# Optimization experiments

Hardware: AMD Instinct MI355X
Metric: run time of the kernel (lower is better)

The kernel has to match this reference:

```python
import jax, jax.numpy as jnp
import numpy as np

B, N, D, H, DH = 1, 1024, 512, 16, 32
NBINS, KIT = 68, 20
NEG = jnp.float32(-1e9)


def _ln(x, g, b):
    mu = jnp.mean(x, -1, keepdims=True)
    var = jnp.mean((x - mu) ** 2, -1, keepdims=True)
    return (x - mu) * jax.lax.rsqrt(var + 1e-5) * g + b


def _heads(x, W):
    b, n, _ = x.shape
    return (x @ W).reshape(b, n, H, DH).transpose(0, 2, 1, 3)  # (B,H,N,DH)


def _forward(h, x_res, pos_bins, mask, ln_mha_g, ln_mha_b, w_q, w_k, w_v, w_g, w_o,
             pos_w, ln_ff_g, ln_ff_b, sw_w1, sw_w3, sw_w2, ln_sink_g, ln_sink_b,
             w_q_sink, w_k_sink, alpha_h, r_h, eps, ln_gate_g, ln_gate_b,
             w_gate_w, w_gate_b, lambda_h_raw):
    b, n, d = h.shape
    mcol = mask[:, None, None, :] > 0  # key-side mask (B,1,1,N)
    mrow = mask[:, None, :, None] > 0

    # ---- MHA with positional bias (flash_diff_attn reference math) ----
    h_n = _ln(h, ln_mha_g, ln_mha_b)
    Q = _heads(h_n, w_q)
    K = _heads(h_n, w_k)
    V = _heads(h_n, w_v)
    G = h_n @ w_g  # (B,N,D) gate, per-head view is equivalent flattened
    bias = pos_w[pos_bins].transpose(0, 3, 1, 2)  # (B,N,N,H) -> (B,H,N,N)
    logits = jnp.einsum('bhnd,bhmd->bhnm', Q, K) / np.float32(np.sqrt(DH)) + bias
    logits = jnp.where(mcol, logits, NEG)
    P = jax.nn.softmax(logits, axis=-1)
    att = jnp.einsum('bhnm,bhmd->bhnd', P, V).transpose(0, 2, 1, 3).reshape(b, n, d)
    h = h + jax.nn.sigmoid(G) * (att @ w_o) * mask[..., None]

    # ---- SwiGLU FFN ----
    h_f = _ln(h, ln_ff_g, ln_ff_b)
    ff = (jax.nn.silu(h_f @ sw_w1) * (h_f @ sw_w3)) @ sw_w2
    h = h + ff * mask[..., None]

    # ---- Balanced Sinkhorn OT transport over coordinates ----
    h_s = _ln(h, ln_sink_g, ln_sink_b)
    Qs = _heads(h_s, w_q_sink)
    Ks = _heads(h_s, w_k_sink)
    Qs = Qs / jnp.clip(jnp.linalg.norm(Qs, axis=-1, keepdims=True), 1e-12)
    Ks = Ks / jnp.clip(jnp.linalg.norm(Ks, axis=-1, keepdims=True), 1e-12)
    sim = jnp.einsum('bhnd,bhmd->bhnm', Qs, Ks)  # cosine similarity
    # Gibbs log-kernel: higher (r_h*sim + alpha_h) => lower cost, scaled by per-head eps
    logKmat = (r_h[:, None, None] * sim + alpha_h[:, None, None]) / eps[:, None, None]
    logKmat = jnp.where(mcol, logKmat, NEG)
    logKmat = jnp.where(mrow, logKmat, NEG)
    n_valid = jnp.sum(mask, -1, keepdims=True)  # (B,1)
    log_a = jnp.where(mask > 0, -jnp.log(n_valid), NEG)[:, None, :]  # (B,1,N) uniform marginal

    def sink_step(carry, _):
        f, g = carry
        f = log_a - jax.nn.logsumexp(logKmat + g[..., None, :], axis=-1)
        g = log_a - jax.nn.logsumexp(logKmat + f[..., None], axis=-2)
        return (f, g), None

    f0 = jnp.zeros((b, H, n), h.dtype)
    (f, g), _ = jax.lax.scan(sink_step, (f0, f0), None, length=KIT)
    logP = f[..., None] + logKmat + g[..., None, :]
    Pn = jax.nn.softmax(logP, axis=-1)  # barycentric row-normalized plan
    x_cent = jnp.einsum('bhnm,bmc->bhnc', Pn, x_res)  # (B,H,N,3)
    vec_h = x_cent - x_res[:, None]

    gate = jax.nn.sigmoid(_ln(h, ln_gate_g, ln_gate_b) @ w_gate_w + w_gate_b)  # (B,N,1)
    lam = (jnp.tanh(lambda_h_raw) / H).reshape(1, H, 1, 1)
    disp = jnp.sum(lam * vec_h, axis=1)  # (B,N,3)
    x_out = x_res + gate * disp * mask[..., None]
    return h, x_out


def setup_inputs() -> dict:
    key = jax.random.key(0)
    ks = jax.random.split(key, 16)
    w = lambda k, s: (0.02 * jax.random.normal(k, s)).astype(jnp.float32)
    nr = H // 4
    return {
        'h': jax.random.normal(ks[0], (B, N, D), jnp.float32),
        'x_res': jax.random.normal(ks[1], (B, N, 3), jnp.float32),
        'pos_bins': jax.random.randint(ks[2], (B, N, N), 0, NBINS),
        'mask': jnp.ones((B, N), jnp.float32),
        'ln_mha_g': jnp.ones(D), 'ln_mha_b': jnp.zeros(D),
        'w_q': w(ks[3], (D, D)), 'w_k': w(ks[4], (D, D)), 'w_v': w(ks[5], (D, D)),
        'w_g': w(ks[6], (D, D)), 'w_o': w(ks[7], (D, D)),
        'pos_w': w(ks[8], (NBINS, H)),
        'ln_ff_g': jnp.ones(D), 'ln_ff_b': jnp.zeros(D),
        'sw_w1': w(ks[9], (D, 4 * D)), 'sw_w3': w(ks[10], (D, 4 * D)),
        'sw_w2': w(ks[11], (4 * D, D)),
        'ln_sink_g': jnp.ones(D), 'ln_sink_b': jnp.zeros(D),
        'w_q_sink': w(ks[12], (D, D)), 'w_k_sink': w(ks[13], (D, D)),
        'alpha_h': jnp.full((H,), -1.0, jnp.float32),
        'r_h': jnp.full((H,), 10.0, jnp.float32),
        'eps': jnp.asarray([0.5] * nr + [1.0] * nr + [2.0] * nr + [4.0] * nr, jnp.float32),
        'ln_gate_g': jnp.ones(D), 'ln_gate_b': jnp.zeros(D),
        'w_gate_w': w(ks[14], (D, 1)), 'w_gate_b': jnp.zeros(1),
        'lambda_h_raw': jnp.zeros(H, jnp.float32),
    }


def reference(h, x_res, pos_bins, mask, ln_mha_g, ln_mha_b, w_q, w_k, w_v, w_g, w_o,
              pos_w, ln_ff_g, ln_ff_b, sw_w1, sw_w3, sw_w2, ln_sink_g, ln_sink_b,
              w_q_sink, w_k_sink, alpha_h, r_h, eps, ln_gate_g, ln_gate_b,
              w_gate_w, w_gate_b, lambda_h_raw):
    return _forward(h, x_res, pos_bins, mask, ln_mha_g, ln_mha_b, w_q, w_k, w_v, w_g,
                    w_o, pos_w, ln_ff_g, ln_ff_b, sw_w1, sw_w3, sw_w2, ln_sink_g,
                    ln_sink_b, w_q_sink, w_k_sink, alpha_h, r_h, eps, ln_gate_g,
                    ln_gate_b, w_gate_w, w_gate_b, lambda_h_raw)
```

## Files before the change

### kernel.cpp

```cpp
#include <hip/hip_runtime.h>
#include <hip/hip_bf16.h>
#include <hip/hip_fp16.h>
#include <math.h>

#define NTOK 1024
#define DMODEL 512
#define NHEAD 16
#define DHEAD 32
#define DFF 2048
#define NBINS 68
#define KIT 20
#define NEGV (-1e9f)
#define NEGH (-30000.0f)

typedef __attribute__((ext_vector_type(8))) short bf16x8;
typedef __attribute__((ext_vector_type(4))) float f32x4;
typedef __attribute__((ext_vector_type(8))) unsigned short u16x8;

__device__ inline unsigned short f2bf(float f) {
    unsigned int u = __float_as_uint(f);
    unsigned int r = (u + 0x7fff + ((u >> 16) & 1)) >> 16;
    return (unsigned short)r;
}

__device__ inline float wave_max64(float v) {
    #pragma unroll
    for (int s = 32; s; s >>= 1) v = fmaxf(v, __shfl_xor(v, s, 64));
    return v;
}
__device__ inline float wave_sum64(float v) {
    #pragma unroll
    for (int s = 32; s; s >>= 1) v += __shfl_xor(v, s, 64);
    return v;
}

__global__ void prep_kernel(const float* __restrict__ w_q, const float* __restrict__ w_k,
                            const float* __restrict__ w_v, const float* __restrict__ w_g,
                            const float* __restrict__ w_o, const float* __restrict__ w_qs,
                            const float* __restrict__ w_ks, const float* __restrict__ sw1,
                            const float* __restrict__ sw3, const float* __restrict__ sw2,
                            unsigned short* __restrict__ wt_qkvg, unsigned short* __restrict__ wt_o,
                            unsigned short* __restrict__ wt_qsks, unsigned short* __restrict__ wt_13,
                            unsigned short* __restrict__ wt_2,
                            const float* __restrict__ mask, float* __restrict__ nv,
                            float* __restrict__ la, float* __restrict__ gv) {
    __shared__ float red[256];
    __shared__ float T[32][33];
    int b = blockIdx.x, tid = threadIdx.x;
    if (b >= 4864) {
        red[tid] = mask[tid] + mask[tid + 256] + mask[tid + 512] + mask[tid + 768];
        __syncthreads();
        for (int off = 128; off; off >>= 1) { if (tid < off) red[tid] += red[tid + off]; __syncthreads(); }
        float lognv = __logf(red[0]);
        if (tid == 0) nv[0] = red[0];
        for (int i = tid; i < NTOK; i += 256) la[i] = (mask[i] > 0.f) ? -lognv : NEGV;
        for (int i = tid; i < NHEAD * NTOK; i += 256) gv[i] = 0.f;
        return;
    }
    const float* W; unsigned short* D; int K, N, t;
    if (b < 1792) {
        int which = b >> 8; t = b & 255; K = 512; N = 512;
        switch (which) {
            case 0: W = w_q;  D = wt_qkvg; break;
            case 1: W = w_k;  D = wt_qkvg + 512 * 512; break;
            case 2: W = w_v;  D = wt_qkvg + 2 * 512 * 512; break;
            case 3: W = w_g;  D = wt_qkvg + 3 * 512 * 512; break;
            case 4: W = w_o;  D = wt_o; break;
            case 5: W = w_qs; D = wt_qsks; break;
            default: W = w_ks; D = wt_qsks + 512 * 512; break;
        }
    } else if (b < 2816) { W = sw1; D = wt_13;              K = 512;  N = 2048; t = b - 1792; }
    else if (b < 3840)   { W = sw3; D = wt_13 + 2048 * 512; K = 512;  N = 2048; t = b - 2816; }
    else                 { W = sw2; D = wt_2;               K = 2048; N = 512;  t = b - 3840; }
    int nx = N >> 5;
    int n0 = (t % nx) * 32, k0 = (t / nx) * 32;
    int r = tid >> 3, c0 = (tid & 7) * 4;
    float4 v4 = *(const float4*)&W[(size_t)(k0 + r) * N + n0 + c0];
    T[r][c0] = v4.x; T[r][c0 + 1] = v4.y; T[r][c0 + 2] = v4.z; T[r][c0 + 3] = v4.w;
    __syncthreads();
    ushort4 o;
    o.x = f2bf(T[c0][r]); o.y = f2bf(T[c0 + 1][r]);
    o.z = f2bf(T[c0 + 2][r]); o.w = f2bf(T[c0 + 3][r]);
    *(ushort4*)&D[(size_t)(n0 + r) * K + k0 + c0] = o;
}

__global__ void ln_bf16_kernel(const float* __restrict__ x, const float* __restrict__ gm,
                               const float* __restrict__ bt, unsigned short* __restrict__ out) {
    int n = blockIdx.x;
    int tid = threadIdx.x;
    __shared__ float red[256];
    const float* row = x + (size_t)n * DMODEL;
    float a = row[tid], b = row[tid + 256];
    red[tid] = a + b;
    __syncthreads();
    for (int off = 128; off; off >>= 1) { if (tid < off) red[tid] += red[tid + off]; __syncthreads(); }
    float mu = red[0] * (1.0f / DMODEL);
    __syncthreads();
    float d0 = a - mu, d1 = b - mu;
    red[tid] = d0 * d0 + d1 * d1;
    __syncthreads();
    for (int off = 128; off; off >>= 1) { if (tid < off) red[tid] += red[tid + off]; __syncthreads(); }
    float rstd = rsqrtf(red[0] * (1.0f / DMODEL) + 1e-5f);
    out[(size_t)n * DMODEL + tid]       = f2bf(d0 * rstd * gm[tid] + bt[tid]);
    out[(size_t)n * DMODEL + tid + 256] = f2bf(d1 * rstd * gm[tid + 256] + bt[tid + 256]);
}

template<int GATED>
__global__ void res_ln_kernel(const float* __restrict__ base, const __half* __restrict__ Gh,
                              const float* __restrict__ t1, const float* __restrict__ mask,
                              const float* __restrict__ gm, const float* __restrict__ bt,
                              float* __restrict__ hout, unsigned short* __restrict__ lnout) {
    int n = blockIdx.x, tid = threadIdx.x;
    __shared__ float red[256];
    float mk = mask[n];
    size_t off = (size_t)n * DMODEL;
    float a, b;
    if (GATED) {
        float g0 = __half2float(Gh[off + tid]);
        float g1 = __half2float(Gh[off + tid + 256]);
        a = base[off + tid]       + g0 * t1[off + tid]       * mk;
        b = base[off + tid + 256] + g1 * t1[off + tid + 256] * mk;
    } else {
        a = base[off + tid]       + t1[off + tid]       * mk;
        b = base[off + tid + 256] + t1[off + tid + 256] * mk;
    }
    hout[off + tid] = a; hout[off + tid + 256] = b;
    red[tid] = a + b;
    __syncthreads();
    for (int o2 = 128; o2; o2 >>= 1) { if (tid < o2) red[tid] += red[tid + o2]; __syncthreads(); }
    float mu = red[0] * (1.0f / DMODEL);
    __syncthreads();
    float d0 = a - mu, d1 = b - mu;
    red[tid] = d0 * d0 + d1 * d1;
    __syncthreads();
    for (int o2 = 128; o2; o2 >>= 1) { if (tid < o2) red[tid] += red[tid + o2]; __syncthreads(); }
    float rstd = rsqrtf(red[0] * (1.0f / DMODEL) + 1e-5f);
    lnout[off + tid]       = f2bf(d0 * rstd * gm[tid] + bt[tid]);
    lnout[off + tid + 256] = f2bf(d1 * rstd * gm[tid + 256] + bt[tid + 256]);
}

template<int MODE>
__global__ __launch_bounds__(256)
void mfma_gemm(const unsigned short* __restrict__ A, const unsigned short* __restrict__ Bt,
               float* __restrict__ C, __half* __restrict__ Ch, unsigned short* __restrict__ Cb,
               unsigned short* __restrict__ P2, unsigned short* __restrict__ P3,
               int N, int K, int lda, int ldb, int ldc,
               long sA, long sB, long sC,
               const float* __restrict__ alpha, const float* __restrict__ epsv,
               const float* __restrict__ mask) {
    __shared__ unsigned short As[128 * 64];
    __shared__ unsigned short Bs[128 * 64];
    const int h = blockIdx.z;
    A += (size_t)h * sA; Bt += (size_t)h * sB;
    const int tid = threadIdx.x;
    const int lane = tid & 63, wid = tid >> 6;
    const int wr = wid >> 1, wc = wid & 1;
    const int lr = lane & 15, kg = lane >> 4;
    const int row0 = blockIdx.y * 128, col0 = blockIdx.x * 128;
    f32x4 acc[4][4];
    #pragma unroll
    for (int i = 0; i < 4; i++)
        #pragma unroll
        for (int j = 0; j < 4; j++) acc[i][j] = (f32x4){0.f, 0.f, 0.f, 0.f};

    for (int k0 = 0; k0 < K; k0 += 64) {
        #pragma unroll
        for (int i = 0; i < 4; i++) {
            int cid = tid + i * 256;
            int r = cid >> 3, sl = cid & 7;
            int rb = col0 + r; if (rb > N - 1) rb = N - 1;
            u16x8 va = *(const u16x8*)&A[(size_t)(row0 + r) * lda + k0 + sl * 8];
            u16x8 vb = *(const u16x8*)&Bt[(size_t)rb * ldb + k0 + sl * 8];
            *(u16x8*)&As[r * 64 + ((sl ^ (r & 7)) * 8)] = va;
            *(u16x8*)&Bs[r * 64 + ((sl ^ (r & 7)) * 8)] = vb;
        }
        __syncthreads();
        #pragma unroll
        for (int ks = 0; ks < 2; ks++) {
            bf16x8 af[4], bfr[4];
            #pragma unroll
            for (int f = 0; f < 4; f++) {
                int ra = wr * 64 + f * 16 + lr;
                af[f] = *(const bf16x8*)&As[ra * 64 + (((ks * 4 + kg) ^ (ra & 7)) * 8)];
                int rb = wc * 64 + f * 16 + lr;
                bfr[f] = *(const bf16x8*)&Bs[rb * 64 + (((ks * 4 + kg) ^ (rb & 7)) * 8)];
            }
            #pragma unroll
            for (int i = 0; i < 4; i++)
                #pragma unroll
                for (int j = 0; j < 4; j++)
                    acc[i][j] = __builtin_amdgcn_mfma_f32_16x16x32_bf16(af[i], bfr[j], acc[i][j], 0, 0, 0);
        }
        __syncthreads();
    }
    float beta = 0.f;
    if (MODE == 1) beta = alpha[h] / epsv[h];
    #pragma unroll
    for (int i = 0; i < 4; i++) {
        int row = row0 + wr * 64 + i * 16 + kg * 4;
        #pragma unroll
        for (int j = 0; j < 4; j++) {
            int col = col0 + wc * 64 + j * 16 + lr;
            #pragma unroll
            for (int e = 0; e < 4; e++) {
                float v = acc[i][j][e];
                if (MODE == 0) {
                    C[(size_t)h * sC + (size_t)(row + e) * ldc + col] = v;
                } else if (MODE == 1) {
                    v += beta;
                    if (!(mask[row + e] > 0.f) || !(mask[col] > 0.f)) v = NEGH;
                    Ch[(size_t)h * sC + (size_t)(row + e) * ldc + col] = __float2half(v);
                } else if (MODE == 2) {
                    if (col < N)
                        Cb[(size_t)h * sC + (size_t)(row + e) * ldc + col] = f2bf(v);
                } else if (MODE == 3) {
                    Ch[(size_t)h * sC + (size_t)(row + e) * ldc + col] = __float2half(v);
                } else {
                    int region = col >> 9;
                    int cc = col & 511;
                    int hh = cc >> 5, kk = cc & 31;
                    if (region == 0) {
                        size_t bidx = (((size_t)hh << 10) + (row + e)) * 64 + kk;
                        Cb[bidx] = f2bf(v * 0.17677669529663687f);
                        Cb[bidx + 32] = 0;
                    } else if (region == 1) {
                        size_t bidx = (((size_t)hh << 10) + (row + e)) * 64 + kk;
                        P2[bidx] = f2bf(v);
                        P2[bidx + 32] = 0;
                    } else if (region == 2) {
                        P3[(((size_t)hh * 32 + kk) << 10) + (row + e)] = f2bf(v);
                    } else {
                        Ch[(size_t)(row + e) * 512 + cc] = __float2half(1.f / (1.f + __expf(-v)));
                    }
                }
            }
        }
    }
}

__global__ __launch_bounds__(256)
void ffn13_gemm(const unsigned short* __restrict__ A, const unsigned short* __restrict__ B1,
                const unsigned short* __restrict__ B2, unsigned short* __restrict__ outb) {
    __shared__ unsigned short As[128 * 64];
    __shared__ unsigned short B1s[128 * 64];
    __shared__ unsigned short B2s[128 * 64];
    const int tid = threadIdx.x;
    const int lane = tid & 63, wid = tid >> 6;
    const int wr = wid >> 1, wc = wid & 1;
    const int lr = lane & 15, kg = lane >> 4;
    const int row0 = blockIdx.y * 128, col0 = blockIdx.x * 128;
    f32x4 acc1[4][4], acc2[4][4];
    #pragma unroll
    for (int i = 0; i < 4; i++)
        #pragma unroll
        for (int j = 0; j < 4; j++) { acc1[i][j] = (f32x4){0,0,0,0}; acc2[i][j] = (f32x4){0,0,0,0}; }
    for (int k0 = 0; k0 < 512; k0 += 64) {
        #pragma unroll
        for (int i = 0; i < 4; i++) {
            int cid = tid + i * 256;
            int r = cid >> 3, sl = cid & 7;
            u16x8 va = *(const u16x8*)&A[(size_t)(row0 + r) * 512 + k0 + sl * 8];
            u16x8 v1 = *(const u16x8*)&B1[(size_t)(col0 + r) * 512 + k0 + sl * 8];
            u16x8 v2 = *(const u16x8*)&B2[(size_t)(col0 + r) * 512 + k0 + sl * 8];
            *(u16x8*)&As[r * 64 + ((sl ^ (r & 7)) * 8)] = va;
            *(u16x8*)&B1s[r * 64 + ((sl ^ (r & 7)) * 8)] = v1;
            *(u16x8*)&B2s[r * 64 + ((sl ^ (r & 7)) * 8)] = v2;
        }
        __syncthreads();
        #pragma unroll
        for (int ks = 0; ks < 2; ks++) {
            bf16x8 af[4], b1f[4], b2f[4];
            #pragma unroll
            for (int f = 0; f < 4; f++) {
                int ra = wr * 64 + f * 16 + lr;
                af[f] = *(const bf16x8*)&As[ra * 64 + (((ks * 4 + kg) ^ (ra & 7)) * 8)];
                int rb = wc * 64 + f * 16 + lr;
                b1f[f] = *(const bf16x8*)&B1s[rb * 64 + (((ks * 4 + kg) ^ (rb & 7)) * 8)];
                b2f[f] = *(const bf16x8*)&B2s[rb * 64 + (((ks * 4 + kg) ^ (rb & 7)) * 8)];
            }
            #pragma unroll
            for (int i = 0; i < 4; i++)
                #pragma unroll
                for (int j = 0; j < 4; j++) {
                    acc1[i][j] = __builtin_amdgcn_mfma_f32_16x16x32_bf16(af[i], b1f[j], acc1[i][j], 0, 0, 0);
                    acc2[i][j] = __builtin_amdgcn_mfma_f32_16x16x32_bf16(af[i], b2f[j], acc2[i][j], 0, 0, 0);
                }
        }
        __syncthreads();
    }
    #pragma unroll
    for (int i = 0; i < 4; i++) {
        int row = row0 + wr * 64 + i * 16 + kg * 4;
        #pragma unroll
        for (int j = 0; j < 4; j++) {
            int col = col0 + wc * 64 + j * 16 + lr;
            #pragma unroll
            for (int e = 0; e < 4; e++) {
                float x = acc1[i][j][e], y = acc2[i][j][e];
                outb[(size_t)(row + e) * 2048 + col] = f2bf(x / (1.f + __expf(-x)) * y);
            }
        }
    }
}

__global__ __launch_bounds__(256)
void bias_softmax_kernel(__half* __restrict__ S, const int* __restrict__ pos_bins,
                         const float* __restrict__ pos_w, const float* __restrict__ mask) {
    __shared__ int   bins_s[NTOK];
    __shared__ float pw_s[NBINS * NHEAD];
    int n = blockIdx.x, tid = threadIdx.x;
    int lane = tid & 63, wid = tid >> 6;
    #pragma unroll
    for (int i = 0; i < 4; i++) {
        int m = tid + i * 256;
        int b = pos_bins[(size_t)n * NTOK + m];
        bins_s[m] = (mask[m] > 0.f) ? b : -1;
    }
    #pragma unroll
    for (int i = 0; i < 5; i++) {
        int idx = tid + i * 256;
        if (idx < NBINS * NHEAD) pw_s[idx] = pos_w[idx];
    }
    __syncthreads();
    int mb = lane * 16;
    #pragma unroll
    for (int hh = 0; hh < 4; hh++) {
        int h = wid * 4 + hh;
        __half* row = S + ((size_t)h * NTOK + n) * NTOK;
        uint4 ua = ((const uint4*)row)[lane * 2];
        uint4 ub = ((const uint4*)row)[lane * 2 + 1];
        unsigned uu[8] = {ua.x, ua.y, ua.z, ua.w, ub.x, ub.y, ub.z, ub.w};
        float v[16];
        #pragma unroll
        for (int j = 0; j < 8; j++) {
            float2 f = __half22float2(*(__half2*)&uu[j]);
            v[2 * j] = f.x; v[2 * j + 1] = f.y;
        }
        float mx = -INFINITY;
        #pragma unroll
        for (int j = 0; j < 16; j++) {
            int b = bins_s[mb + j];
            v[j] = (b >= 0) ? v[j] + pw_s[b * NHEAD + h] : NEGV;
            mx = fmaxf(mx, v[j]);
        }
        mx = wave_max64(mx);
        float sum = 0.f;
        #pragma unroll
        for (int j = 0; j < 16; j++) { v[j] = __expf(v[j] - mx); sum += v[j]; }
        float inv = 1.f / wave_sum64(sum);
        unsigned short o[16];
        #pragma unroll
        for (int j = 0; j < 16; j++) o[j] = f2bf(v[j] * inv);
        ((uint4*)row)[lane * 2]     = *(uint4*)&o[0];
        ((uint4*)row)[lane * 2 + 1] = *(uint4*)&o[8];
    }
}

__global__ void norm_pad_kernel(const float* __restrict__ qsks, const float* __restrict__ rh,
                                const float* __restrict__ ev,
                                unsigned short* __restrict__ Qp, unsigned short* __restrict__ Kp) {
    int idx = blockIdx.x * 256 + threadIdx.x;
    int h = idx >> 10, n = idx & 1023;
    const float* q = &qsks[(size_t)n * 1024 + h * 32];
    const float* k = q + 512;
    float s = rh[h] / ev[h];
    float qv[32], kv[32];
    float ssq = 0.f, ssk = 0.f;
    #pragma unroll
    for (int d = 0; d < 32; d++) {
        qv[d] = q[d]; ssq += qv[d] * qv[d];
        kv[d] = k[d]; ssk += kv[d] * kv[d];
    }
    float iq = s / fmaxf(sqrtf(ssq), 1e-12f);
    float ik = 1.f / fmaxf(sqrtf(ssk), 1e-12f);
    size_t base = (size_t)idx * 64;
    #pragma unroll
    for (int d = 0; d < 32; d++) {
        Qp[base + d] = f2bf(qv[d] * iq);
        Kp[base + d] = f2bf(kv[d] * ik);
        Qp[base + 32 + d] = 0;
        Kp[base + 32 + d] = 0;
    }
}

__global__ __launch_bounds__(256)
void sink_pass_kernel(const __half* __restrict__ Sb, const float* __restrict__ dual,
                      const float* __restrict__ la, float* __restrict__ outv) {
    int tid = threadIdx.x, lane = tid & 63, wid = tid >> 6;
    int row0 = blockIdx.x * 8;
    int h = row0 >> 10;
    const float4* dp = (const float4*)(dual + ((size_t)h << 10));
    float dv[16];
    *(float4*)&dv[0]  = dp[lane * 4];     *(float4*)&dv[4]  = dp[lane * 4 + 1];
    *(float4*)&dv[8]  = dp[lane * 4 + 2]; *(float4*)&dv[12] = dp[lane * 4 + 3];
    #pragma unroll
    for (int r = 0; r < 2; r++) {
        int row = row0 + wid * 2 + r;
        const uint4* sp = (const uint4*)(Sb + ((size_t)row << 10));
        uint4 ua = sp[lane * 2], ub = sp[lane * 2 + 1];
        unsigned uu[8] = {ua.x, ua.y, ua.z, ua.w, ub.x, ub.y, ub.z, ub.w};
        float v[16];
        #pragma unroll
        for (int j = 0; j < 8; j++) {
            float2 f = __half22float2(*(__half2*)&uu[j]);
            v[2 * j] = f.x; v[2 * j + 1] = f.y;
        }
        float mx = -INFINITY;
        #pragma unroll
        for (int j = 0; j < 16; j++) { v[j] += dv[j]; mx = fmaxf(mx, v[j]); }
        mx = wave_max64(mx);
        float sum = 0.f;
        #pragma unroll
        for (int j = 0; j < 16; j++) sum += __expf(v[j] - mx);
        sum = wave_sum64(sum);
        if (lane == 0) outv[row] = la[row & 1023] - (mx + __logf(sum));
    }
}

__global__ __launch_bounds__(256)
void transport_kernel(const __half* __restrict__ Sb, const float* __restrict__ f,
                      const float* __restrict__ g, const float* __restrict__ x_res,
                      float* __restrict__ xc) {
    int tid = threadIdx.x, lane = tid & 63, wid = tid >> 6;
    int row0 = blockIdx.x * 8;
    int h = row0 >> 10;
    const float4* gp = (const float4*)(g + ((size_t)h << 10));
    float gv[16];
    *(float4*)&gv[0]  = gp[lane * 4];     *(float4*)&gv[4]  = gp[lane * 4 + 1];
    *(float4*)&gv[8]  = gp[lane * 4 + 2]; *(float4*)&gv[12] = gp[lane * 4 + 3];
    float4 xv[12];
    const float4* xp = (const float4*)x_res + lane * 12;
    #pragma unroll
    for (int k = 0; k < 12; k++) xv[k] = xp[k];
    const float* xf = (const float*)xv;
    #pragma unroll
    for (int r = 0; r < 2; r++) {
        int row = row0 + wid * 2 + r;
        float fr = f[row];
        const uint4* sp = (const uint4*)(Sb + ((size_t)row << 10));
        uint4 ua = sp[lane * 2], ub = sp[lane * 2 + 1];
        unsigned uu[8] = {ua.x, ua.y, ua.z, ua.w, ub.x, ub.y, ub.z, ub.w};
        float v[16];
        #pragma unroll
        for (int j = 0; j < 8; j++) {
            float2 fx = __half22float2(*(__half2*)&uu[j]);
            v[2 * j] = fx.x; v[2 * j + 1] = fx.y;
        }
        float mx = -INFINITY;
        #pragma unroll
        for (int j = 0; j < 16; j++) { v[j] += fr + gv[j]; mx = fmaxf(mx, v[j]); }
        mx = wave_max64(mx);
        float sum = 0.f, a0 = 0.f, a1 = 0.f, a2 = 0.f;
        #pragma unroll
        for (int j = 0; j < 16; j++) {
            float e = __expf(v[j] - mx);
            sum += e;
            a0 += e * xf[3 * j];
            a1 += e * xf[3 * j + 1];
            a2 += e * xf[3 * j + 2];
        }
        sum = wave_sum64(sum);
        a0 = wave_sum64(a0); a1 = wave_sum64(a1); a2 = wave_sum64(a2);
        if (lane == 0) {
            float inv = 1.f / sum;
            xc[(size_t)row * 3 + 0] = a0 * inv;
            xc[(size_t)row * 3 + 1] = a1 * inv;
            xc[(size_t)row * 3 + 2] = a2 * inv;
        }
    }
}

__global__ void final_kernel(const float* __restrict__ h2, const float* __restrict__ x_res,
                             const float* __restrict__ mask, const float* __restrict__ gm,
                             const float* __restrict__ bt, const float* __restrict__ wg,
                             const float* __restrict__ wb, const float* __restrict__ lamraw,
                             const float* __restrict__ xc, float* __restrict__ xout) {
    int n = blockIdx.x;
    int tid = threadIdx.x;
    __shared__ float red[256];
    const float* row = h2 + (size_t)n * DMODEL;
    float a = row[tid], b = row[tid + 256];
    red[tid] = a + b;
    __syncthreads();
    for (int off = 128; off; off >>= 1) { if (tid < off) red[tid] += red[tid + off]; __syncthreads(); }
    float mu = red[0] * (1.0f / DMODEL);
    __syncthreads();
    float d0 = a - mu, d1 = b - mu;
    red[tid] = d0 * d0 + d1 * d1;
    __syncthreads();
    for (int off = 128; off; off >>= 1) { if (tid < off) red[tid] += red[tid + off]; __syncthreads(); }
    float rstd = rsqrtf(red[0] * (1.0f / DMODEL) + 1e-5f);
    __syncthreads();
    float t0 = (d0 * rstd * gm[tid] + bt[tid]) * wg[tid];
    float t1 = (d1 * rstd * gm[tid + 256] + bt[tid + 256]) * wg[tid + 256];
    red[tid] = t0 + t1;
    __syncthreads();
    for (int off = 128; off; off >>= 1) { if (tid < off) red[tid] += red[tid + off]; __syncthreads(); }
    if (tid == 0) {
        float gate = 1.f / (1.f + expf(-(red[0] + wb[0])));
        float mk = mask[n];
        #pragma unroll
        for (int c = 0; c < 3; c++) {
            float xr = x_res[n * 3 + c];
            float disp = 0.f;
            for (int h = 0; h < NHEAD; h++) {
                float lam = tanhf(lamraw[h]) * (1.f / NHEAD);
                disp += lam * (xc[((size_t)h * NTOK + n) * 3 + c] - xr);
            }
            xout[n * 3 + c] = xr + gate * disp * mk;
        }
    }
}

extern "C" void kernel_launch(void* const* d_in, const int* in_sizes, int n_in,
                              void* d_out, int out_size, void* d_ws, size_t ws_size,
                              hipStream_t stream) {
    const float* h          = (const float*)d_in[0];
    const float* x_res      = (const float*)d_in[1];
    const int*   pos_bins   = (const int*)d_in[2];
    const float* mask       = (const float*)d_in[3];
    const float* ln_mha_g   = (const float*)d_in[4];
    const float* ln_mha_b   = (const float*)d_in[5];
    const float* w_q        = (const float*)d_in[6];
    const float* w_k        = (const float*)d_in[7];
    const float* w_v        = (const float*)d_in[8];
    const float* w_g        = (const float*)d_in[9];
    const float* w_o        = (const float*)d_in[10];
    const float* pos_w      = (const float*)d_in[11];
    const float* ln_ff_g    = (const float*)d_in[12];
    const float* ln_ff_b    = (const float*)d_in[13];
    const float* sw_w1      = (const float*)d_in[14];
    const float* sw_w3      = (const float*)d_in[15];
    const float* sw_w2      = (const float*)d_in[16];
    const float* ln_sink_g  = (const float*)d_in[17];
    const float* ln_sink_b  = (const float*)d_in[18];
    const float* w_q_sink   = (const float*)d_in[19];
    const float* w_k_sink   = (const float*)d_in[20];
    const float* alpha_h    = (const float*)d_in[21];
    const float* r_h        = (const float*)d_in[22];
    const float* eps        = (const float*)d_in[23];
    const float* ln_gate_g  = (const float*)d_in[24];
    const float* ln_gate_b  = (const float*)d_in[25];
    const float* w_gate_w   = (const float*)d_in[26];
    const float* w_gate_b   = (const float*)d_in[27];
    const float* lambda_raw = (const float*)d_in[28];
    float* out = (float*)d_out;
    const size_t ND = (size_t)NTOK * DMODEL;

    char* Wp = (char*)d_ws;
    auto alloc = [&](size_t bytes) { char* p = Wp; Wp += (bytes + 255) & ~(size_t)255; return p; };
    unsigned short* wt_qkvg = (unsigned short*)alloc((size_t)2048 * 512 * 2);
    unsigned short* wt_o    = (unsigned short*)alloc((size_t)512 * 512 * 2);
    unsigned short* wt_13   = (unsigned short*)alloc((size_t)4096 * 512 * 2);
    unsigned short* wt_2    = (unsigned short*)alloc((size_t)512 * 2048 * 2);
    unsigned short* wt_qsks = (unsigned short*)alloc((size_t)1024 * 512 * 2);
    unsigned short* hnb     = (unsigned short*)alloc(ND * 2);
    __half*         Gh      = (__half*)alloc(ND * 2);
    unsigned short* attb    = (unsigned short*)alloc(ND * 2);
    float*          t1      = (float*)alloc(ND * 4);
    float*          h1      = (float*)alloc(ND * 4);
    unsigned short* ffb     = (unsigned short*)alloc((size_t)1024 * 2048 * 2);
    unsigned short* Qp      = (unsigned short*)alloc((size_t)16 * 1024 * 64 * 2);
    unsigned short* Kp      = (unsigned short*)alloc((size_t)16 * 1024 * 64 * 2);
    unsigned short* Vt      = (unsigned short*)alloc((size_t)16 * 32 * 1024 * 2);
    float*          qsks    = (float*)alloc((size_t)1024 * 1024 * 4);
    char*           R       = alloc((size_t)64 * 1024 * 1024);
    float*          fv      = (float*)alloc((size_t)16 * 1024 * 4);
    float*          gv      = (float*)alloc((size_t)16 * 1024 * 4);
    float*          la      = (float*)alloc((size_t)1024 * 4);
    float*          xc      = (float*)alloc((size_t)16 * 1024 * 3 * 4);
    float*          nv      = (float*)alloc(256);

    __half* Sh_att = (__half*)R;
    __half* Sh     = (__half*)R;
    __half* Sth    = (__half*)(R + (size_t)32 * 1024 * 1024);

    prep_kernel<<<4865, 256, 0, stream>>>(w_q, w_k, w_v, w_g, w_o, w_q_sink, w_k_sink,
                                          sw_w1, sw_w3, sw_w2,
                                          wt_qkvg, wt_o, wt_qsks, wt_13, wt_2,
                                          mask, nv, la, gv);

    ln_bf16_kernel<<<NTOK, 256, 0, stream>>>(h, ln_mha_g, ln_mha_b, hnb);
    mfma_gemm<4><<<dim3(16, 8, 1), 256, 0, stream>>>(hnb, wt_qkvg, nullptr, Gh, Qp, Kp, Vt,
        2048, 512, 512, 512, 2048, 0, 0, 0, nullptr, nullptr, nullptr);
    mfma_gemm<3><<<dim3(8, 8, 16), 256, 0, stream>>>(Qp, Kp, nullptr, Sh_att, nullptr, nullptr, nullptr,
        1024, 64, 64, 64, 1024, 65536, 65536, 1048576, nullptr, nullptr, nullptr);
    bias_softmax_kernel<<<NTOK, 256, 0, stream>>>(Sh_att, pos_bins, pos_w, mask);
    mfma_gemm<2><<<dim3(1, 8, 16), 256, 0, stream>>>((const unsigned short*)Sh_att, Vt,
        nullptr, nullptr, attb, nullptr, nullptr,
        32, 1024, 1024, 1024, 512, 1048576, 32768, 32, nullptr, nullptr, nullptr);
    mfma_gemm<0><<<dim3(4, 8, 1), 256, 0, stream>>>(attb, wt_o, t1, nullptr, nullptr, nullptr, nullptr,
        512, 512, 512, 512, 512, 0, 0, 0, nullptr, nullptr, nullptr);
    res_ln_kernel<1><<<NTOK, 256, 0, stream>>>(h, Gh, t1, mask, ln_ff_g, ln_ff_b, h1, hnb);

    ffn13_gemm<<<dim3(16, 8), 256, 0, stream>>>(hnb, wt_13, wt_13 + 2048 * 512, ffb);
    mfma_gemm<0><<<dim3(4, 8, 1), 256, 0, stream>>>(ffb, wt_2, t1, nullptr, nullptr, nullptr, nullptr,
        512, 2048, 2048, 2048, 512, 0, 0, 0, nullptr, nullptr, nullptr);
    res_ln_kernel<0><<<NTOK, 256, 0, stream>>>(h1, nullptr, t1, mask, ln_sink_g, ln_sink_b, out, hnb);

    mfma_gemm<0><<<dim3(8, 8, 1), 256, 0, stream>>>(hnb, wt_qsks, qsks, nullptr, nullptr, nullptr, nullptr,
        1024, 512, 512, 512, 1024, 0, 0, 0, nullptr, nullptr, nullptr);
    norm_pad_kernel<<<64, 256, 0, stream>>>(qsks, r_h, eps, Qp, Kp);
    mfma_gemm<1><<<dim3(8, 8, 16), 256, 0, stream>>>(Qp, Kp, nullptr, Sh, nullptr, nullptr, nullptr,
        1024, 64, 64, 64, 1024, 65536, 65536, 1048576, alpha_h, eps, mask);
    mfma_gemm<1><<<dim3(8, 8, 16), 256, 0, stream>>>(Kp, Qp, nullptr, Sth, nullptr, nullptr, nullptr,
        1024, 64, 64, 64, 1024, 65536, 65536, 1048576, alpha_h, eps, mask);

    for (int it = 0; it < KIT; it++) {
        sink_pass_kernel<<<2048, 256, 0, stream>>>(Sh,  gv, la, fv);
        sink_pass_kernel<<<2048, 256, 0, stream>>>(Sth, fv, la, gv);
    }
    transport_kernel<<<2048, 256, 0, stream>>>(Sh, fv, gv, x_res, xc);

    final_kernel<<<NTOK, 256, 0, stream>>>(out, x_res, mask, ln_gate_g, ln_gate_b,
                                           w_gate_w, w_gate_b, lambda_raw, xc, out + ND);
}
```

Measured before the change: 700.7 us.

## Recompute Sinkhorn kernel on the fly via MFMA instead of materializing fp16 matrices

```diff
diff --git a/kernel.cpp b/kernel.cpp
--- a/kernel.cpp
+++ b/kernel.cpp
@@ -42,19 +42,39 @@
                             unsigned short* __restrict__ wt_qkvg, unsigned short* __restrict__ wt_o,
                             unsigned short* __restrict__ wt_qsks, unsigned short* __restrict__ wt_13,
                             unsigned short* __restrict__ wt_2,
-                            const float* __restrict__ mask, float* __restrict__ nv,
-                            float* __restrict__ la, float* __restrict__ gv) {
+                            const float* __restrict__ mask, float* __restrict__ la,
+                            float* __restrict__ gv,
+                            const float* __restrict__ hin, const float* __restrict__ lng,
+                            const float* __restrict__ lnb, unsigned short* __restrict__ hnb) {
     __shared__ float red[256];
     __shared__ float T[32][33];
     int b = blockIdx.x, tid = threadIdx.x;
-    if (b >= 4864) {
+    if (b == 4864) {
         red[tid] = mask[tid] + mask[tid + 256] + mask[tid + 512] + mask[tid + 768];
         __syncthreads();
         for (int off = 128; off; off >>= 1) { if (tid < off) red[tid] += red[tid + off]; __syncthreads(); }
         float lognv = __logf(red[0]);
-        if (tid == 0) nv[0] = red[0];
         for (int i = tid; i < NTOK; i += 256) la[i] = (mask[i] > 0.f) ? -lognv : NEGV;
-        for (int i = tid; i < NHEAD * NTOK; i += 256) gv[i] = 0.f;
+        for (int i = tid; i < NHEAD * NTOK; i += 256)
+            gv[i] = (mask[i & 1023] > 0.f) ? 0.f : NEGV;
+        return;
+    }
+    if (b > 4864) {
+        int n = b - 4865;
+        const float* row = hin + (size_t)n * DMODEL;
+        float a = row[tid], bb = row[tid + 256];
+        red[tid] = a + bb;
+        __syncthreads();
+        for (int off = 128; off; off >>= 1) { if (tid < off) red[tid] += red[tid + off]; __syncthreads(); }
+        float mu = red[0] * (1.0f / DMODEL);
+        __syncthreads();
+        float d0 = a - mu, d1 = bb - mu;
+        red[tid] = d0 * d0 + d1 * d1;
+        __syncthreads();
+        for (int off = 128; off; off >>= 1) { if (tid < off) red[tid] += red[tid + off]; __syncthreads(); }
+        float rstd = rsqrtf(red[0] * (1.0f / DMODEL) + 1e-5f);
+        hnb[(size_t)n * DMODEL + tid]       = f2bf(d0 * rstd * lng[tid] + lnb[tid]);
+        hnb[(size_t)n * DMODEL + tid + 256] = f2bf(d1 * rstd * lng[tid + 256] + lnb[tid + 256]);
         return;
     }
     const float* W; unsigned short* D; int K, N, t;
@@ -82,27 +102,6 @@
     o.x = f2bf(T[c0][r]); o.y = f2bf(T[c0 + 1][r]);
     o.z = f2bf(T[c0 + 2][r]); o.w = f2bf(T[c0 + 3][r]);
     *(ushort4*)&D[(size_t)(n0 + r) * K + k0 + c0] = o;
-}
-
-__global__ void ln_bf16_kernel(const float* __restrict__ x, const float* __restrict__ gm,
-                               const float* __restrict__ bt, unsigned short* __restrict__ out) {
-    int n = blockIdx.x;
-    int tid = threadIdx.x;
-    __shared__ float red[256];
-    const float* row = x + (size_t)n * DMODEL;
-    float a = row[tid], b = row[tid + 256];
-    red[tid] = a + b;
-    __syncthreads();
-    for (int off = 128; off; off >>= 1) { if (tid < off) red[tid] += red[tid + off]; __syncthreads(); }
-    float mu = red[0] * (1.0f / DMODEL);
-    __syncthreads();
-    float d0 = a - mu, d1 = b - mu;
-    red[tid] = d0 * d0 + d1 * d1;
-    __syncthreads();
-    for (int off = 128; off; off >>= 1) { if (tid < off) red[tid] += red[tid + off]; __syncthreads(); }
-    float rstd = rsqrtf(red[0] * (1.0f / DMODEL) + 1e-5f);
-    out[(size_t)n * DMODEL + tid]       = f2bf(d0 * rstd * gm[tid] + bt[tid]);
-    out[(size_t)n * DMODEL + tid + 256] = f2bf(d1 * rstd * gm[tid + 256] + bt[tid + 256]);
 }
 
 template<int GATED>
@@ -145,12 +144,10 @@
                float* __restrict__ C, __half* __restrict__ Ch, unsigned short* __restrict__ Cb,
                unsigned short* __restrict__ P2, unsigned short* __restrict__ P3,
                int N, int K, int lda, int ldb, int ldc,
-               long sA, long sB, long sC,
-               const float* __restrict__ alpha, const float* __restrict__ epsv,
-               const float* __restrict__ mask) {
+               long sA, long sB, long sC) {
     __shared__ unsigned short As[128 * 64];
     __shared__ unsigned short Bs[128 * 64];
-    const int h = blockIdx.z;
+    int h = blockIdx.z;
     A += (size_t)h * sA; Bt += (size_t)h * sB;
     const int tid = threadIdx.x;
     const int lane = tid & 63, wid = tid >> 6;
@@ -193,8 +190,6 @@
         }
         __syncthreads();
     }
-    float beta = 0.f;
-    if (MODE == 1) beta = alpha[h] / epsv[h];
     #pragma unroll
     for (int i = 0; i < 4; i++) {
         int row = row0 + wr * 64 + i * 16 + kg * 4;
@@ -206,10 +201,6 @@
                 float v = acc[i][j][e];
                 if (MODE == 0) {
                     C[(size_t)h * sC + (size_t)(row + e) * ldc + col] = v;
-                } else if (MODE == 1) {
-                    v += beta;
-                    if (!(mask[row + e] > 0.f) || !(mask[col] > 0.f)) v = NEGH;
-                    Ch[(size_t)h * sC + (size_t)(row + e) * ldc + col] = __float2half(v);
                 } else if (MODE == 2) {
                     if (col < N)
                         Cb[(size_t)h * sC + (size_t)(row + e) * ldc + col] = f2bf(v);
@@ -358,7 +349,7 @@
 
 __global__ void norm_pad_kernel(const float* __restrict__ qsks, const float* __restrict__ rh,
                                 const float* __restrict__ ev,
-                                unsigned short* __restrict__ Qp, unsigned short* __restrict__ Kp) {
+                                unsigned short* __restrict__ Qsc, unsigned short* __restrict__ Ksc) {
     int idx = blockIdx.x * 256 + threadIdx.x;
     int h = idx >> 10, n = idx & 1023;
     const float* q = &qsks[(size_t)n * 1024 + h * 32];
@@ -373,99 +364,97 @@
     }
     float iq = s / fmaxf(sqrtf(ssq), 1e-12f);
     float ik = 1.f / fmaxf(sqrtf(ssk), 1e-12f);
-    size_t base = (size_t)idx * 64;
+    size_t base = (size_t)idx * 32;
     #pragma unroll
     for (int d = 0; d < 32; d++) {
-        Qp[base + d] = f2bf(qv[d] * iq);
-        Kp[base + d] = f2bf(kv[d] * ik);
-        Qp[base + 32 + d] = 0;
-        Kp[base + 32 + d] = 0;
-    }
-}
-
+        Qsc[base + d] = f2bf(qv[d] * iq);
+        Ksc[base + d] = f2bf(kv[d] * ik);
+    }
+}
+
+template<int TRANSPORT>
 __global__ __launch_bounds__(256)
-void sink_pass_kernel(const __half* __restrict__ Sb, const float* __restrict__ dual,
-                      const float* __restrict__ la, float* __restrict__ outv) {
-    int tid = threadIdx.x, lane = tid & 63, wid = tid >> 6;
-    int row0 = blockIdx.x * 8;
-    int h = row0 >> 10;
-    const float4* dp = (const float4*)(dual + ((size_t)h << 10));
-    float dv[16];
-    *(float4*)&dv[0]  = dp[lane * 4];     *(float4*)&dv[4]  = dp[lane * 4 + 1];
-    *(float4*)&dv[8]  = dp[lane * 4 + 2]; *(float4*)&dv[12] = dp[lane * 4 + 3];
-    #pragma unroll
-    for (int r = 0; r < 2; r++) {
-        int row = row0 + wid * 2 + r;
-        const uint4* sp = (const uint4*)(Sb + ((size_t)row << 10));
-        uint4 ua = sp[lane * 2], ub = sp[lane * 2 + 1];
-        unsigned uu[8] = {ua.x, ua.y, ua.z, ua.w, ub.x, ub.y, ub.z, ub.w};
-        float v[16];
-        #pragma unroll
-        for (int j = 0; j < 8; j++) {
-            float2 f = __half22float2(*(__half2*)&uu[j]);
-            v[2 * j] = f.x; v[2 * j + 1] = f.y;
-        }
-        float mx = -INFINITY;
-        #pragma unroll
-        for (int j = 0; j < 16; j++) { v[j] += dv[j]; mx = fmaxf(mx, v[j]); }
-        mx = wave_max64(mx);
-        float sum = 0.f;
-        #pragma unroll
-        for (int j = 0; j < 16; j++) sum += __expf(v[j] - mx);
-        sum = wave_sum64(sum);
-        if (lane == 0) outv[row] = la[row & 1023] - (mx + __logf(sum));
-    }
-}
-
-__global__ __launch_bounds__(256)
-void transport_kernel(const __half* __restrict__ Sb, const float* __restrict__ f,
-                      const float* __restrict__ g, const float* __restrict__ x_res,
-                      float* __restrict__ xc) {
-    int tid = threadIdx.x, lane = tid & 63, wid = tid >> 6;
-    int row0 = blockIdx.x * 8;
-    int h = row0 >> 10;
-    const float4* gp = (const float4*)(g + ((size_t)h << 10));
-    float gv[16];
-    *(float4*)&gv[0]  = gp[lane * 4];     *(float4*)&gv[4]  = gp[lane * 4 + 1];
-    *(float4*)&gv[8]  = gp[lane * 4 + 2]; *(float4*)&gv[12] = gp[lane * 4 + 3];
-    float4 xv[12];
-    const float4* xp = (const float4*)x_res + lane * 12;
-    #pragma unroll
-    for (int k = 0; k < 12; k++) xv[k] = xp[k];
-    const float* xf = (const float*)xv;
-    #pragma unroll
-    for (int r = 0; r < 2; r++) {
-        int row = row0 + wid * 2 + r;
-        float fr = f[row];
-        const uint4* sp = (const uint4*)(Sb + ((size_t)row << 10));
-        uint4 ua = sp[lane * 2], ub = sp[lane * 2 + 1];
-        unsigned uu[8] = {ua.x, ua.y, ua.z, ua.w, ub.x, ub.y, ub.z, ub.w};
-        float v[16];
-        #pragma unroll
-        for (int j = 0; j < 8; j++) {
-            float2 fx = __half22float2(*(__half2*)&uu[j]);
-            v[2 * j] = fx.x; v[2 * j + 1] = fx.y;
-        }
-        float mx = -INFINITY;
-        #pragma unroll
-        for (int j = 0; j < 16; j++) { v[j] += fr + gv[j]; mx = fmaxf(mx, v[j]); }
-        mx = wave_max64(mx);
-        float sum = 0.f, a0 = 0.f, a1 = 0.f, a2 = 0.f;
-        #pragma unroll
-        for (int j = 0; j < 16; j++) {
-            float e = __expf(v[j] - mx);
-            sum += e;
-            a0 += e * xf[3 * j];
-            a1 += e * xf[3 * j + 1];
-            a2 += e * xf[3 * j + 2];
-        }
-        sum = wave_sum64(sum);
-        a0 = wave_sum64(a0); a1 = wave_sum64(a1); a2 = wave_sum64(a2);
-        if (lane == 0) {
-            float inv = 1.f / sum;
-            xc[(size_t)row * 3 + 0] = a0 * inv;
-            xc[(size_t)row * 3 + 1] = a1 * inv;
-            xc[(size_t)row * 3 + 2] = a2 * inv;
+void sink_fused_kernel(const unsigned short* __restrict__ Arows,
+                       const unsigned short* __restrict__ Bcols,
+                       const float* __restrict__ dual, const float* __restrict__ frow,
+                       const float* __restrict__ la,
+                       const float* __restrict__ alpha, const float* __restrict__ epsv,
+                       const float* __restrict__ x_res,
+                       float* __restrict__ outv, float* __restrict__ xc) {
+    __shared__ float part[4][16][4];
+    const int tid = threadIdx.x, lane = tid & 63, w = tid >> 6;
+    const int b = blockIdx.x;
+    const int h = b >> 6, row0 = (b & 63) << 4;
+    const float bet = alpha[h] / epsv[h];
+    const size_t hb = (size_t)h << 10;
+    bf16x8 af = *(const bf16x8*)&Arows[(hb + row0 + (lane & 15)) * 32 + (lane >> 4) * 8];
+    float fr[4];
+    if (TRANSPORT) {
+        float4 f4 = *(const float4*)&frow[hb + row0 + (lane >> 4) * 4];
+        fr[0] = f4.x; fr[1] = f4.y; fr[2] = f4.z; fr[3] = f4.w;
+    }
+    const int wbase = w << 8;
+    float s[4] = {0.f, 0.f, 0.f, 0.f};
+    float a0[4] = {0.f, 0.f, 0.f, 0.f}, a1[4] = {0.f, 0.f, 0.f, 0.f}, a2[4] = {0.f, 0.f, 0.f, 0.f};
+    #pragma unroll
+    for (int t = 0; t < 16; t++) {
+        int col = wbase + t * 16 + (lane & 15);
+        bf16x8 bf = *(const bf16x8*)&Bcols[(hb + col) * 32 + (lane >> 4) * 8];
+        f32x4 acc = (f32x4){0.f, 0.f, 0.f, 0.f};
+        acc = __builtin_amdgcn_mfma_f32_16x16x32_bf16(af, bf, acc, 0, 0, 0);
+        float gcol = dual[hb + col];
+        float x0, x1, x2;
+        if (TRANSPORT) {
+            const float* xr = x_res + col * 3;
+            x0 = xr[0]; x1 = xr[1]; x2 = xr[2];
+        }
+        #pragma unroll
+        for (int e = 0; e < 4; e++) {
+            float v = acc[e] + bet + gcol;
+            if (TRANSPORT) v += fr[e];
+            float ev = __expf(v);
+            s[e] += ev;
+            if (TRANSPORT) { a0[e] += ev * x0; a1[e] += ev * x1; a2[e] += ev * x2; }
+        }
+    }
+    #pragma unroll
+    for (int off = 1; off < 16; off <<= 1) {
+        #pragma unroll
+        for (int e = 0; e < 4; e++) {
+            s[e] += __shfl_xor(s[e], off, 64);
+            if (TRANSPORT) {
+                a0[e] += __shfl_xor(a0[e], off, 64);
+                a1[e] += __shfl_xor(a1[e], off, 64);
+                a2[e] += __shfl_xor(a2[e], off, 64);
+            }
+        }
+    }
+    if ((lane & 15) == 0) {
+        int rg = (lane >> 4) * 4;
+        #pragma unroll
+        for (int e = 0; e < 4; e++) {
+            part[w][rg + e][0] = s[e];
+            if (TRANSPORT) {
+                part[w][rg + e][1] = a0[e];
+                part[w][rg + e][2] = a1[e];
+                part[w][rg + e][3] = a2[e];
+            }
+        }
+    }
+    __syncthreads();
+    if (tid < 16) {
+        float tot = part[0][tid][0] + part[1][tid][0] + part[2][tid][0] + part[3][tid][0];
+        int row = row0 + tid;
+        if (!TRANSPORT) {
+            outv[hb + row] = la[row] - __logf(fmaxf(tot, 1e-38f));
+        } else {
+            float inv = 1.f / fmaxf(tot, 1e-38f);
+            float b0 = part[0][tid][1] + part[1][tid][1] + part[2][tid][1] + part[3][tid][1];
+            float b1 = part[0][tid][2] + part[1][tid][2] + part[2][tid][2] + part[3][tid][2];
+            float b2 = part[0][tid][3] + part[1][tid][3] + part[2][tid][3] + part[3][tid][3];
+            xc[(hb + row) * 3 + 0] = b0 * inv;
+            xc[(hb + row) * 3 + 1] = b1 * inv;
+            xc[(hb + row) * 3 + 2] = b2 * inv;
         }
     }
 }
@@ -563,54 +552,52 @@
     unsigned short* Qp      = (unsigned short*)alloc((size_t)16 * 1024 * 64 * 2);
     unsigned short* Kp      = (unsigned short*)alloc((size_t)16 * 1024 * 64 * 2);
     unsigned short* Vt      = (unsigned short*)alloc((size_t)16 * 32 * 1024 * 2);
+    unsigned short* Qsc     = (unsigned short*)alloc((size_t)16 * 1024 * 32 * 2);
+    unsigned short* Ksc     = (unsigned short*)alloc((size_t)16 * 1024 * 32 * 2);
     float*          qsks    = (float*)alloc((size_t)1024 * 1024 * 4);
-    char*           R       = alloc((size_t)64 * 1024 * 1024);
+    char*           R       = alloc((size_t)32 * 1024 * 1024);
     float*          fv      = (float*)alloc((size_t)16 * 1024 * 4);
     float*          gv      = (float*)alloc((size_t)16 * 1024 * 4);
     float*          la      = (float*)alloc((size_t)1024 * 4);
     float*          xc      = (float*)alloc((size_t)16 * 1024 * 3 * 4);
-    float*          nv      = (float*)alloc(256);
 
     __half* Sh_att = (__half*)R;
-    __half* Sh     = (__half*)R;
-    __half* Sth    = (__half*)(R + (size_t)32 * 1024 * 1024);
-
-    prep_kernel<<<4865, 256, 0, stream>>>(w_q, w_k, w_v, w_g, w_o, w_q_sink, w_k_sink,
+
+    prep_kernel<<<5889, 256, 0, stream>>>(w_q, w_k, w_v, w_g, w_o, w_q_sink, w_k_sink,
                                           sw_w1, sw_w3, sw_w2,
                                           wt_qkvg, wt_o, wt_qsks, wt_13, wt_2,
-                                          mask, nv, la, gv);
-
-    ln_bf16_kernel<<<NTOK, 256, 0, stream>>>(h, ln_mha_g, ln_mha_b, hnb);
+                                          mask, la, gv,
+                                          h, ln_mha_g, ln_mha_b, hnb);
+
     mfma_gemm<4><<<dim3(16, 8, 1), 256, 0, stream>>>(hnb, wt_qkvg, nullptr, Gh, Qp, Kp, Vt,
-        2048, 512, 512, 512, 2048, 0, 0, 0, nullptr, nullptr, nullptr);
+        2048, 512, 512, 512, 2048, 0, 0, 0);
     mfma_gemm<3><<<dim3(8, 8, 16), 256, 0, stream>>>(Qp, Kp, nullptr, Sh_att, nullptr, nullptr, nullptr,
-        1024, 64, 64, 64, 1024, 65536, 65536, 1048576, nullptr, nullptr, nullptr);
+        1024, 64, 64, 64, 1024, 65536, 65536, 1048576);
     bias_softmax_kernel<<<NTOK, 256, 0, stream>>>(Sh_att, pos_bins, pos_w, mask);
     mfma_gemm<2><<<dim3(1, 8, 16), 256, 0, stream>>>((const unsigned short*)Sh_att, Vt,
         nullptr, nullptr, attb, nullptr, nullptr,
-        32, 1024, 1024, 1024, 512, 1048576, 32768, 32, nullptr, nullptr, nullptr);
+        32, 1024, 1024, 1024, 512, 1048576, 32768, 32);
     mfma_gemm<0><<<dim3(4, 8, 1), 256, 0, stream>>>(attb, wt_o, t1, nullptr, nullptr, nullptr, nullptr,
-        512, 512, 512, 512, 512, 0, 0, 0, nullptr, nullptr, nullptr);
+        512, 512, 512, 512, 512, 0, 0, 0);
     res_ln_kernel<1><<<NTOK, 256, 0, stream>>>(h, Gh, t1, mask, ln_ff_g, ln_ff_b, h1, hnb);
 
     ffn13_gemm<<<dim3(16, 8), 256, 0, stream>>>(hnb, wt_13, wt_13 + 2048 * 512, ffb);
     mfma_gemm<0><<<dim3(4, 8, 1), 256, 0, stream>>>(ffb, wt_2, t1, nullptr, nullptr, nullptr, nullptr,
-        512, 2048, 2048, 2048, 512, 0, 0, 0, nullptr, nullptr, nullptr);
+        512, 2048, 2048, 2048, 512, 0, 0, 0);
     res_ln_kernel<0><<<NTOK, 256, 0, stream>>>(h1, nullptr, t1, mask, ln_sink_g, ln_sink_b, out, hnb);
 
     mfma_gemm<0><<<dim3(8, 8, 1), 256, 0, stream>>>(hnb, wt_qsks, qsks, nullptr, nullptr, nullptr, nullptr,
-        1024, 512, 512, 512, 1024, 0, 0, 0, nullptr, nullptr, nullptr);
-    norm_pad_kernel<<<64, 256, 0, stream>>>(qsks, r_h, eps, Qp, Kp);
-    mfma_gemm<1><<<dim3(8, 8, 16), 256, 0, stream>>>(Qp, Kp, nullptr, Sh, nullptr, nullptr, nullptr,
-        1024, 64, 64, 64, 1024, 65536, 65536, 1048576, alpha_h, eps, mask);
-    mfma_gemm<1><<<dim3(8, 8, 16), 256, 0, stream>>>(Kp, Qp, nullptr, Sth, nullptr, nullptr, nullptr,
-        1024, 64, 64, 64, 1024, 65536, 65536, 1048576, alpha_h, eps, mask);
+        1024, 512, 512, 512, 1024, 0, 0, 0);
+    norm_pad_kernel<<<64, 256, 0, stream>>>(qsks, r_h, eps, Qsc, Ksc);
 
     for (int it = 0; it < KIT; it++) {
-        sink_pass_kernel<<<2048, 256, 0, stream>>>(Sh,  gv, la, fv);
-        sink_pass_kernel<<<2048, 256, 0, stream>>>(Sth, fv, la, gv);
-    }
-    transport_kernel<<<2048, 256, 0, stream>>>(Sh, fv, gv, x_res, xc);
+        sink_fused_kernel<0><<<1024, 256, 0, stream>>>(Qsc, Ksc, gv, nullptr, la,
+                                                       alpha_h, eps, nullptr, fv, nullptr);
+        sink_fused_kernel<0><<<1024, 256, 0, stream>>>(Ksc, Qsc, fv, nullptr, la,
+                                                       alpha_h, eps, nullptr, gv, nullptr);
+    }
+    sink_fused_kernel<1><<<1024, 256, 0, stream>>>(Qsc, Ksc, gv, fv, la,
+                                                   alpha_h, eps, x_res, nullptr, xc);
 
     final_kernel<<<NTOK, 256, 0, stream>>>(out, x_res, mask, ln_gate_g, ln_gate_b,
                                            w_gate_w, w_gate_b, lambda_raw, xc, out + ND);
```

Result: faster. 607.2 us (-13.3%).
